# Optimization experiments

Hardware: AMD Instinct MI355X
Metric: run time of the kernel (lower is better)

Reference implementation:

```python
import jax, jax.numpy as jnp
import numpy as np

B, H, KV, HD, D, S = 8, 32, 8, 128, 4096, 4096
PAST = S - 2  # 4094, cache nearly full
ROPE_THETA = 10000.0


def rotate_half(x):
    h = x.shape[-1] // 2
    return jnp.concatenate([-x[..., h:], x[..., :h]], axis=-1)


def setup_inputs() -> dict:
    key = jax.random.key(0)
    ks = jax.random.split(key, 10)
    hidden_states = jax.random.normal(ks[0], (B, 1, D), jnp.float32)
    # HF additive causal mask for decode: 0 where position is valid, -inf-ish beyond
    pos = jnp.arange(S)
    attention_mask = jnp.broadcast_to(
        jnp.where(pos < PAST + 1, 0.0, -1e9).astype(jnp.float32)[None, None, None, :],
        (B, 1, 1, S),
    )
    # RoPE cos/sin for the single decoded position (position id = PAST)
    inv_freq = 1.0 / (ROPE_THETA ** (jnp.arange(0, HD, 2, dtype=jnp.float32) / HD))
    ang = PAST * inv_freq  # [HD/2]
    emb = jnp.concatenate([ang, ang], axis=-1)  # [HD]
    cos = jnp.broadcast_to(jnp.cos(emb)[None, None, :], (B, 1, HD)).astype(jnp.float32)
    sin = jnp.broadcast_to(jnp.sin(emb)[None, None, :], (B, 1, HD)).astype(jnp.float32)
    past_key = jax.random.normal(ks[1], (B, KV, PAST, HD), jnp.float32)
    past_value = jax.random.normal(ks[2], (B, KV, PAST, HD), jnp.float32)
    k_cache = jax.random.normal(ks[3], (B, KV, S, HD), jnp.float32)
    v_cache = jax.random.normal(ks[4], (B, KV, S, HD), jnp.float32)
    Wq = jax.random.normal(ks[5], (D, H * HD), jnp.float32) * 0.02
    Wk = jax.random.normal(ks[6], (D, KV * HD), jnp.float32) * 0.02
    Wv = jax.random.normal(ks[7], (D, KV * HD), jnp.float32) * 0.02
    Wo = jax.random.normal(ks[8], (H * HD, D), jnp.float32) * 0.02
    return dict(hidden_states=hidden_states, attention_mask=attention_mask, cos=cos,
                sin=sin, past_key=past_key, past_value=past_value,
                k_cache=k_cache, v_cache=v_cache, Wq=Wq, Wk=Wk, Wv=Wv, Wo=Wo)


def reference(hidden_states, attention_mask, cos, sin, past_key, past_value,
              k_cache, v_cache, Wq, Wk, Wv, Wo):
    b = hidden_states.shape[0]
    past_len = past_key.shape[2]  # static
    # q/k/v projections for the single decode token
    q = (hidden_states @ Wq).reshape(b, 1, H, HD).transpose(0, 2, 1, 3)   # [B,H,1,hd]
    k = (hidden_states @ Wk).reshape(b, 1, KV, HD).transpose(0, 2, 1, 3)  # [B,KV,1,hd]
    v = (hidden_states @ Wv).reshape(b, 1, KV, HD).transpose(0, 2, 1, 3)
    # rotary: cos/sin [B,1,hd] -> unsqueeze head dim -> [B,1,1,hd]
    c = cos[:, None, :, :]
    s = sin[:, None, :, :]
    q = q * c + rotate_half(q) * s
    k = k * c + rotate_half(k) * s
    # StaticCache: scatter past K/V into positions [0, past_len), new token at past_len
    kf = k_cache.at[:, :, :past_len, :].set(past_key)
    kf = kf.at[:, :, past_len:past_len + 1, :].set(k)
    vf = v_cache.at[:, :, :past_len, :].set(past_value)
    vf = vf.at[:, :, past_len:past_len + 1, :].set(v)
    # GQA: repeat kv heads
    n_rep = H // KV
    kr = jnp.repeat(kf, n_rep, axis=1)  # [B,H,S,hd]
    vr = jnp.repeat(vf, n_rep, axis=1)
    scores = jnp.einsum('bhqd,bhkd->bhqk', q, kr) / np.float32(np.sqrt(HD))
    scores = scores + attention_mask  # [B,1,1,S] broadcasts over heads
    probs = jax.nn.softmax(scores.astype(jnp.float32), axis=-1).astype(q.dtype)
    out = jnp.einsum('bhqk,bhkd->bhqd', probs, vr)  # [B,H,1,hd]
    out = out.transpose(0, 2, 1, 3).reshape(b, 1, H * HD)
    return out @ Wo  # [B,1,D]
```

## Files before the change

kernel.cpp:

```cpp
#include <hip/hip_runtime.h>

#define BB 8
#define HH 32
#define KVH 8
#define HD 128
#define DD 4096
#define PAST 4094
#define QCOLS 4096
#define KVCOLS 1024
#define NC_QKV 6144
#define DCH 64
#define NDCH 64
#define CHUNK 64
#define NCHUNK 64
#define QSCALE 0.08838834764831845f

__global__ __launch_bounds__(256)
void matvec_partial(const float* __restrict__ hin,
                    const float* __restrict__ W0,
                    const float* __restrict__ W1,
                    const float* __restrict__ W2,
                    int c_w1, int c_w2, int NC,
                    float* __restrict__ part)
{
    __shared__ float hl[DCH][BB];
    const int tid = threadIdx.x;
    const int d0 = blockIdx.y * DCH;
    const int cb = blockIdx.x * 512;

    for (int idx = tid; idx < DCH * BB; idx += 256) {
        int dd = idx & (DCH - 1);
        int b = idx >> 6;
        hl[dd][b] = hin[b * DD + d0 + dd];
    }
    __syncthreads();

    const int c = cb + tid * 2;
    const float* W;
    int ldw, cl;
    if (c < c_w1)      { W = W0; ldw = c_w1;        cl = c; }
    else if (c < c_w2) { W = W1; ldw = c_w2 - c_w1; cl = c - c_w1; }
    else               { W = W2; ldw = NC - c_w2;   cl = c - c_w2; }
    const float* wp = W + (size_t)d0 * ldw + cl;

    float2 acc[BB];
    #pragma unroll
    for (int b = 0; b < BB; ++b) { acc[b].x = 0.f; acc[b].y = 0.f; }

    #pragma unroll 8
    for (int dd = 0; dd < DCH; ++dd) {
        float2 w = *(const float2*)wp;
        wp += ldw;
        float hv[8];
        *(float4*)&hv[0] = *(const float4*)&hl[dd][0];
        *(float4*)&hv[4] = *(const float4*)&hl[dd][4];
        #pragma unroll
        for (int b = 0; b < BB; ++b) {
            acc[b].x = fmaf(hv[b], w.x, acc[b].x);
            acc[b].y = fmaf(hv[b], w.y, acc[b].y);
        }
    }

    float* po = part + (size_t)blockIdx.y * (BB * NC) + c;
    #pragma unroll
    for (int b = 0; b < BB; ++b) {
        *(float2*)(po + (size_t)b * NC) = acc[b];
    }
}

#define FIN_PER_B 3584
__global__ __launch_bounds__(256)
void qkv_finish(const float* __restrict__ part,
                const float* __restrict__ cosv,
                const float* __restrict__ sinv,
                float* __restrict__ qout,
                float* __restrict__ knew,
                float* __restrict__ vnew)
{
    const int idx = blockIdx.x * 256 + threadIdx.x;
    const int b = idx / FIN_PER_B;
    const int r = idx - b * FIN_PER_B;

    if (r < 2560) {
        const int hd = r & 63;
        const int head = r >> 6;
        const int c_lo = head * HD + hd;
        const float* p0 = part + (size_t)b * NC_QKV + c_lo;
        const float* p1 = p0 + 64;
        float s_lo = 0.f, s_hi = 0.f;
        #pragma unroll 8
        for (int i = 0; i < NDCH; ++i) {
            s_lo += p0[(size_t)i * (BB * NC_QKV)];
            s_hi += p1[(size_t)i * (BB * NC_QKV)];
        }
        const float cs_lo = cosv[b * HD + hd];
        const float sn_lo = sinv[b * HD + hd];
        const float cs_hi = cosv[b * HD + hd + 64];
        const float sn_hi = sinv[b * HD + hd + 64];
        const float v_lo = fmaf(s_lo, cs_lo, -s_hi * sn_lo);
        const float v_hi = fmaf(s_hi, cs_hi,  s_lo * sn_hi);
        if (c_lo < QCOLS) {
            qout[b * QCOLS + c_lo]      = v_lo * QSCALE;
            qout[b * QCOLS + c_lo + 64] = v_hi * QSCALE;
        } else {
            knew[b * KVCOLS + (c_lo - QCOLS)]      = v_lo;
            knew[b * KVCOLS + (c_lo - QCOLS) + 64] = v_hi;
        }
    } else {
        const int c = r - 2560 + QCOLS + KVCOLS;
        const float* p = part + (size_t)b * NC_QKV + c;
        float s = 0.f;
        #pragma unroll 8
        for (int i = 0; i < NDCH; ++i) s += p[(size_t)i * (BB * NC_QKV)];
        vnew[b * KVCOLS + (c - QCOLS - KVCOLS)] = s;
    }
}

__global__ __launch_bounds__(256)
void attn_partial(const float* __restrict__ past_key,
                  const float* __restrict__ past_value,
                  const float* __restrict__ q,
                  const float* __restrict__ knew,
                  const float* __restrict__ vnew,
                  float* __restrict__ pacc,
                  float* __restrict__ pl)
{
    const int pair = blockIdx.x;
    const int wid = threadIdx.x >> 6;
    const int chunk = blockIdx.y * 4 + wid;
    const int b = pair >> 3;
    const int kv = pair & 7;
    const int lane = threadIdx.x & 63;
    const int half = lane >> 5;
    const int lh = lane & 31;

    const float* qb = q + b * QCOLS + (kv * 4) * HD + 4 * lh;
    const float4 qv0 = *(const float4*)(qb);
    const float4 qv1 = *(const float4*)(qb + HD);
    const float4 qv2 = *(const float4*)(qb + 2 * HD);
    const float4 qv3 = *(const float4*)(qb + 3 * HD);

    const float* kb = past_key   + (size_t)pair * PAST * HD;
    const float* vb = past_value + (size_t)pair * PAST * HD;

    float4 acc0 = {0,0,0,0}, acc1 = {0,0,0,0}, acc2 = {0,0,0,0}, acc3 = {0,0,0,0};
    float l0 = 0.f, l1 = 0.f, l2 = 0.f, l3 = 0.f;

    const int jbase = chunk * CHUNK + half;

    if (chunk < NCHUNK - 1) {
        const float* kp = kb + (size_t)jbase * HD + 4 * lh;
        const float* vp = vb + (size_t)jbase * HD + 4 * lh;
        #pragma unroll 4
        for (int it = 0; it < 32; ++it) {
            const float4 kk = *(const float4*)kp;  kp += 2 * HD;
            float s0 = kk.x*qv0.x + kk.y*qv0.y + kk.z*qv0.z + kk.w*qv0.w;
            float s1 = kk.x*qv1.x + kk.y*qv1.y + kk.z*qv1.z + kk.w*qv1.w;
            float s2 = kk.x*qv2.x + kk.y*qv2.y + kk.z*qv2.z + kk.w*qv2.w;
            float s3 = kk.x*qv3.x + kk.y*qv3.y + kk.z*qv3.z + kk.w*qv3.w;
            #pragma unroll
            for (int m = 1; m <= 16; m <<= 1) {
                s0 += __shfl_xor(s0, m, 64);
                s1 += __shfl_xor(s1, m, 64);
                s2 += __shfl_xor(s2, m, 64);
                s3 += __shfl_xor(s3, m, 64);
            }
            const float4 vv = *(const float4*)vp;  vp += 2 * HD;
            const float p0 = __expf(s0);
            const float p1 = __expf(s1);
            const float p2 = __expf(s2);
            const float p3 = __expf(s3);
            l0 += p0; l1 += p1; l2 += p2; l3 += p3;
            acc0.x = fmaf(p0, vv.x, acc0.x); acc0.y = fmaf(p0, vv.y, acc0.y);
            acc0.z = fmaf(p0, vv.z, acc0.z); acc0.w = fmaf(p0, vv.w, acc0.w);
            acc1.x = fmaf(p1, vv.x, acc1.x); acc1.y = fmaf(p1, vv.y, acc1.y);
            acc1.z = fmaf(p1, vv.z, acc1.z); acc1.w = fmaf(p1, vv.w, acc1.w);
            acc2.x = fmaf(p2, vv.x, acc2.x); acc2.y = fmaf(p2, vv.y, acc2.y);
            acc2.z = fmaf(p2, vv.z, acc2.z); acc2.w = fmaf(p2, vv.w, acc2.w);
            acc3.x = fmaf(p3, vv.x, acc3.x); acc3.y = fmaf(p3, vv.y, acc3.y);
            acc3.z = fmaf(p3, vv.z, acc3.z); acc3.w = fmaf(p3, vv.w, acc3.w);
        }
    } else {
        const float* kn = knew + pair * HD;
        const float* vn = vnew + pair * HD;
        #pragma unroll 2
        for (int it = 0; it < 32; ++it) {
            const int j = jbase + it * 2;
            const bool valid = (j <= PAST);
            const float* kp;
            const float* vp;
            if (j < PAST) { kp = kb + (size_t)j * HD; vp = vb + (size_t)j * HD; }
            else          { kp = kn;                   vp = vn; }

            const float4 kk = *(const float4*)(kp + 4 * lh);
            float s0 = kk.x*qv0.x + kk.y*qv0.y + kk.z*qv0.z + kk.w*qv0.w;
            float s1 = kk.x*qv1.x + kk.y*qv1.y + kk.z*qv1.z + kk.w*qv1.w;
            float s2 = kk.x*qv2.x + kk.y*qv2.y + kk.z*qv2.z + kk.w*qv2.w;
            float s3 = kk.x*qv3.x + kk.y*qv3.y + kk.z*qv3.z + kk.w*qv3.w;
            #pragma unroll
            for (int m = 1; m <= 16; m <<= 1) {
                s0 += __shfl_xor(s0, m, 64);
                s1 += __shfl_xor(s1, m, 64);
                s2 += __shfl_xor(s2, m, 64);
                s3 += __shfl_xor(s3, m, 64);
            }
            const float4 vv = *(const float4*)(vp + 4 * lh);
            const float p0 = valid ? __expf(s0) : 0.f;
            const float p1 = valid ? __expf(s1) : 0.f;
            const float p2 = valid ? __expf(s2) : 0.f;
            const float p3 = valid ? __expf(s3) : 0.f;
            l0 += p0; l1 += p1; l2 += p2; l3 += p3;
            acc0.x = fmaf(p0, vv.x, acc0.x); acc0.y = fmaf(p0, vv.y, acc0.y);
            acc0.z = fmaf(p0, vv.z, acc0.z); acc0.w = fmaf(p0, vv.w, acc0.w);
            acc1.x = fmaf(p1, vv.x, acc1.x); acc1.y = fmaf(p1, vv.y, acc1.y);
            acc1.z = fmaf(p1, vv.z, acc1.z); acc1.w = fmaf(p1, vv.w, acc1.w);
            acc2.x = fmaf(p2, vv.x, acc2.x); acc2.y = fmaf(p2, vv.y, acc2.y);
            acc2.z = fmaf(p2, vv.z, acc2.z); acc2.w = fmaf(p2, vv.w, acc2.w);
            acc3.x = fmaf(p3, vv.x, acc3.x); acc3.y = fmaf(p3, vv.y, acc3.y);
            acc3.z = fmaf(p3, vv.z, acc3.z); acc3.w = fmaf(p3, vv.w, acc3.w);
        }
    }

    l0 += __shfl_xor(l0, 32, 64);
    l1 += __shfl_xor(l1, 32, 64);
    l2 += __shfl_xor(l2, 32, 64);
    l3 += __shfl_xor(l3, 32, 64);
    acc0.x += __shfl_xor(acc0.x, 32, 64); acc0.y += __shfl_xor(acc0.y, 32, 64);
    acc0.z += __shfl_xor(acc0.z, 32, 64); acc0.w += __shfl_xor(acc0.w, 32, 64);
    acc1.x += __shfl_xor(acc1.x, 32, 64); acc1.y += __shfl_xor(acc1.y, 32, 64);
    acc1.z += __shfl_xor(acc1.z, 32, 64); acc1.w += __shfl_xor(acc1.w, 32, 64);
    acc2.x += __shfl_xor(acc2.x, 32, 64); acc2.y += __shfl_xor(acc2.y, 32, 64);
    acc2.z += __shfl_xor(acc2.z, 32, 64); acc2.w += __shfl_xor(acc2.w, 32, 64);
    acc3.x += __shfl_xor(acc3.x, 32, 64); acc3.y += __shfl_xor(acc3.y, 32, 64);
    acc3.z += __shfl_xor(acc3.z, 32, 64); acc3.w += __shfl_xor(acc3.w, 32, 64);

    if (half == 0) {
        float* po = pacc + (((size_t)pair * NCHUNK + chunk) * 4) * HD + 4 * lh;
        *(float4*)(po)          = acc0;
        *(float4*)(po + HD)     = acc1;
        *(float4*)(po + 2*HD)   = acc2;
        *(float4*)(po + 3*HD)   = acc3;
        if (lh == 0) {
            float* plo = pl + ((size_t)pair * NCHUNK + chunk) * 4;
            plo[0] = l0; plo[1] = l1; plo[2] = l2; plo[3] = l3;
        }
    }
}

__global__ __launch_bounds__(256)
void attn_combine(const float* __restrict__ pacc,
                  const float* __restrict__ pl,
                  float* __restrict__ attn_out)
{
    const int idx = blockIdx.x * 256 + threadIdx.x;
    const int d = idx & 127;
    const int h = (idx >> 7) & 31;
    const int b = idx >> 12;
    const int kv = h >> 2;
    const int qi = h & 3;
    const int pair = b * 8 + kv;

    const float* pa  = pacc + (((size_t)pair * NCHUNK) * 4 + qi) * HD + d;
    const float* pls = pl + (size_t)pair * NCHUNK * 4 + qi;
    float acc = 0.f, lsum = 0.f;
    #pragma unroll 8
    for (int c = 0; c < NCHUNK; ++c) {
        acc  += pa[(size_t)c * 4 * HD];
        lsum += pls[c * 4];
    }
    attn_out[b * QCOLS + h * HD + d] = acc / lsum;
}

__global__ __launch_bounds__(256)
void wo_finish(const float* __restrict__ part, float* __restrict__ out)
{
    const int idx = blockIdx.x * 256 + threadIdx.x;
    float s = 0.f;
    #pragma unroll 8
    for (int i = 0; i < NDCH; ++i) s += part[(size_t)i * (BB * QCOLS) + idx];
    out[idx] = s;
}

extern "C" void kernel_launch(void* const* d_in, const int* in_sizes, int n_in,
                              void* d_out, int out_size, void* d_ws, size_t ws_size,
                              hipStream_t stream)
{
    (void)in_sizes; (void)n_in; (void)out_size; (void)ws_size;
    const float* hidden     = (const float*)d_in[0];
    const float* cosv       = (const float*)d_in[2];
    const float* sinv       = (const float*)d_in[3];
    const float* past_key   = (const float*)d_in[4];
    const float* past_value = (const float*)d_in[5];
    const float* Wq = (const float*)d_in[8];
    const float* Wk = (const float*)d_in[9];
    const float* Wv = (const float*)d_in[10];
    const float* Wo = (const float*)d_in[11];
    float* out = (float*)d_out;
    float* ws  = (float*)d_ws;

    float* qkv_part = ws;
    float* qrope    = qkv_part + (size_t)NDCH * BB * NC_QKV;
    float* knew     = qrope + BB * QCOLS;
    float* vnew     = knew + BB * KVCOLS;
    float* pacc     = vnew + BB * KVCOLS;
    float* pl       = pacc + (size_t)64 * NCHUNK * 4 * HD;
    float* attn_out = pl + (size_t)64 * NCHUNK * 4;
    float* wo_part  = qkv_part;

    matvec_partial<<<dim3(12, NDCH), 256, 0, stream>>>(
        hidden, Wq, Wk, Wv, 4096, 5120, NC_QKV, qkv_part);
    qkv_finish<<<(BB * FIN_PER_B) / 256, 256, 0, stream>>>(
        qkv_part, cosv, sinv, qrope, knew, vnew);
    attn_partial<<<dim3(64, NCHUNK / 4), 256, 0, stream>>>(
        past_key, past_value, qrope, knew, vnew, pacc, pl);
    attn_combine<<<(BB * HH * HD) / 256, 256, 0, stream>>>(pacc, pl, attn_out);
    matvec_partial<<<dim3(8, NDCH), 256, 0, stream>>>(
        attn_out, Wo, Wo, Wo, 4096, 5120, QCOLS, wo_part);
    wo_finish<<<(BB * QCOLS) / 256, 256, 0, stream>>>(wo_part, out);
}
```

Measured before the change: 111.7 us.

## Halve matvec split-K chunks, DPP reductions, in-block attention chunk combine, vectorized finish

Doubles the D-chunk per matvec block, which halves the number of split-K partials written and re-read. It replaces the shfl_xor reductions in the attention kernel with DPP/swizzle intrinsics. Each attention block now reduces its four wavefront chunks in shared memory before writing one partial, which shrinks the combine pass. wo_finish is vectorized to float4. The costs are fewer matvec blocks in flight, which lowers parallelism, and a new __syncthreads in the attention kernel.

```diff
diff --git a/kernel.cpp b/kernel.cpp
--- a/kernel.cpp
+++ b/kernel.cpp
@@ -9,11 +9,26 @@
 #define QCOLS 4096
 #define KVCOLS 1024
 #define NC_QKV 6144
-#define DCH 64
-#define NDCH 64
+#define DCH 128
+#define NDCH 32
 #define CHUNK 64
-#define NCHUNK 64
+#define YCH 16
 #define QSCALE 0.08838834764831845f
+
+__device__ __forceinline__ float sum32(float x) {
+    int t;
+    t = __builtin_amdgcn_update_dpp(0, __float_as_int(x), 0x121, 0xf, 0xf, false);
+    x += __int_as_float(t);
+    t = __builtin_amdgcn_update_dpp(0, __float_as_int(x), 0x122, 0xf, 0xf, false);
+    x += __int_as_float(t);
+    t = __builtin_amdgcn_update_dpp(0, __float_as_int(x), 0x124, 0xf, 0xf, false);
+    x += __int_as_float(t);
+    t = __builtin_amdgcn_update_dpp(0, __float_as_int(x), 0x128, 0xf, 0xf, false);
+    x += __int_as_float(t);
+    t = __builtin_amdgcn_ds_swizzle(__float_as_int(x), 0x401F);
+    x += __int_as_float(t);
+    return x;
+}
 
 __global__ __launch_bounds__(256)
 void matvec_partial(const float* __restrict__ hin,
@@ -30,7 +45,7 @@
 
     for (int idx = tid; idx < DCH * BB; idx += 256) {
         int dd = idx & (DCH - 1);
-        int b = idx >> 6;
+        int b = idx >> 7;
         hl[dd][b] = hin[b * DD + d0 + dd];
     }
     __syncthreads();
@@ -47,7 +62,7 @@
     #pragma unroll
     for (int b = 0; b < BB; ++b) { acc[b].x = 0.f; acc[b].y = 0.f; }
 
-    #pragma unroll 8
+    #pragma unroll 16
     for (int dd = 0; dd < DCH; ++dd) {
         float2 w = *(const float2*)wp;
         wp += ldw;
@@ -148,7 +163,7 @@
 
     const int jbase = chunk * CHUNK + half;
 
-    if (chunk < NCHUNK - 1) {
+    if (chunk < 63) {
         const float* kp = kb + (size_t)jbase * HD + 4 * lh;
         const float* vp = vb + (size_t)jbase * HD + 4 * lh;
         #pragma unroll 4
@@ -158,13 +173,7 @@
             float s1 = kk.x*qv1.x + kk.y*qv1.y + kk.z*qv1.z + kk.w*qv1.w;
             float s2 = kk.x*qv2.x + kk.y*qv2.y + kk.z*qv2.z + kk.w*qv2.w;
             float s3 = kk.x*qv3.x + kk.y*qv3.y + kk.z*qv3.z + kk.w*qv3.w;
-            #pragma unroll
-            for (int m = 1; m <= 16; m <<= 1) {
-                s0 += __shfl_xor(s0, m, 64);
-                s1 += __shfl_xor(s1, m, 64);
-                s2 += __shfl_xor(s2, m, 64);
-                s3 += __shfl_xor(s3, m, 64);
-            }
+            s0 = sum32(s0); s1 = sum32(s1); s2 = sum32(s2); s3 = sum32(s3);
             const float4 vv = *(const float4*)vp;  vp += 2 * HD;
             const float p0 = __expf(s0);
             const float p1 = __expf(s1);
@@ -197,13 +206,7 @@
             float s1 = kk.x*qv1.x + kk.y*qv1.y + kk.z*qv1.z + kk.w*qv1.w;
             float s2 = kk.x*qv2.x + kk.y*qv2.y + kk.z*qv2.z + kk.w*qv2.w;
             float s3 = kk.x*qv3.x + kk.y*qv3.y + kk.z*qv3.z + kk.w*qv3.w;
-            #pragma unroll
-            for (int m = 1; m <= 16; m <<= 1) {
-                s0 += __shfl_xor(s0, m, 64);
-                s1 += __shfl_xor(s1, m, 64);
-                s2 += __shfl_xor(s2, m, 64);
-                s3 += __shfl_xor(s3, m, 64);
-            }
+            s0 = sum32(s0); s1 = sum32(s1); s2 = sum32(s2); s3 = sum32(s3);
             const float4 vv = *(const float4*)(vp + 4 * lh);
             const float p0 = valid ? __expf(s0) : 0.f;
             const float p1 = valid ? __expf(s1) : 0.f;
@@ -234,16 +237,29 @@
     acc3.x += __shfl_xor(acc3.x, 32, 64); acc3.y += __shfl_xor(acc3.y, 32, 64);
     acc3.z += __shfl_xor(acc3.z, 32, 64); acc3.w += __shfl_xor(acc3.w, 32, 64);
 
+    __shared__ float lacc[4][4][HD];
+    __shared__ float ll[4][4];
     if (half == 0) {
-        float* po = pacc + (((size_t)pair * NCHUNK + chunk) * 4) * HD + 4 * lh;
-        *(float4*)(po)          = acc0;
-        *(float4*)(po + HD)     = acc1;
-        *(float4*)(po + 2*HD)   = acc2;
-        *(float4*)(po + 3*HD)   = acc3;
+        *(float4*)&lacc[wid][0][4 * lh] = acc0;
+        *(float4*)&lacc[wid][1][4 * lh] = acc1;
+        *(float4*)&lacc[wid][2][4 * lh] = acc2;
+        *(float4*)&lacc[wid][3][4 * lh] = acc3;
         if (lh == 0) {
-            float* plo = pl + ((size_t)pair * NCHUNK + chunk) * 4;
-            plo[0] = l0; plo[1] = l1; plo[2] = l2; plo[3] = l3;
-        }
+            ll[wid][0] = l0; ll[wid][1] = l1; ll[wid][2] = l2; ll[wid][3] = l3;
+        }
+    }
+    __syncthreads();
+    const int d2 = lane * 2;
+    float ax = lacc[0][wid][d2]     + lacc[1][wid][d2]
+             + lacc[2][wid][d2]     + lacc[3][wid][d2];
+    float ay = lacc[0][wid][d2 + 1] + lacc[1][wid][d2 + 1]
+             + lacc[2][wid][d2 + 1] + lacc[3][wid][d2 + 1];
+    float* po = pacc + (((size_t)pair * YCH + blockIdx.y) * 4 + wid) * HD + d2;
+    float2 r; r.x = ax; r.y = ay;
+    *(float2*)po = r;
+    if (lane == 0) {
+        pl[((size_t)pair * YCH + blockIdx.y) * 4 + wid] =
+            ll[0][wid] + ll[1][wid] + ll[2][wid] + ll[3][wid];
     }
 }
 
@@ -260,11 +276,11 @@
     const int qi = h & 3;
     const int pair = b * 8 + kv;
 
-    const float* pa  = pacc + (((size_t)pair * NCHUNK) * 4 + qi) * HD + d;
-    const float* pls = pl + (size_t)pair * NCHUNK * 4 + qi;
+    const float* pa  = pacc + ((size_t)pair * YCH * 4 + qi) * HD + d;
+    const float* pls = pl + (size_t)pair * YCH * 4 + qi;
     float acc = 0.f, lsum = 0.f;
     #pragma unroll 8
-    for (int c = 0; c < NCHUNK; ++c) {
+    for (int c = 0; c < YCH; ++c) {
         acc  += pa[(size_t)c * 4 * HD];
         lsum += pls[c * 4];
     }
@@ -275,10 +291,14 @@
 void wo_finish(const float* __restrict__ part, float* __restrict__ out)
 {
     const int idx = blockIdx.x * 256 + threadIdx.x;
-    float s = 0.f;
+    const float* p = part + (size_t)idx * 4;
+    float4 s = {0.f, 0.f, 0.f, 0.f};
     #pragma unroll 8
-    for (int i = 0; i < NDCH; ++i) s += part[(size_t)i * (BB * QCOLS) + idx];
-    out[idx] = s;
+    for (int i = 0; i < NDCH; ++i) {
+        const float4 t = *(const float4*)(p + (size_t)i * (BB * QCOLS));
+        s.x += t.x; s.y += t.y; s.z += t.z; s.w += t.w;
+    }
+    *(float4*)(out + (size_t)idx * 4) = s;
 }
 
 extern "C" void kernel_launch(void* const* d_in, const int* in_sizes, int n_in,
@@ -303,18 +323,18 @@
     float* knew     = qrope + BB * QCOLS;
     float* vnew     = knew + BB * KVCOLS;
     float* pacc     = vnew + BB * KVCOLS;
-    float* pl       = pacc + (size_t)64 * NCHUNK * 4 * HD;
-    float* attn_out = pl + (size_t)64 * NCHUNK * 4;
+    float* pl       = pacc + (size_t)64 * YCH * 4 * HD;
+    float* attn_out = pl + (size_t)64 * YCH * 4;
     float* wo_part  = qkv_part;
 
     matvec_partial<<<dim3(12, NDCH), 256, 0, stream>>>(
         hidden, Wq, Wk, Wv, 4096, 5120, NC_QKV, qkv_part);
     qkv_finish<<<(BB * FIN_PER_B) / 256, 256, 0, stream>>>(
         qkv_part, cosv, sinv, qrope, knew, vnew);
-    attn_partial<<<dim3(64, NCHUNK / 4), 256, 0, stream>>>(
+    attn_partial<<<dim3(64, YCH), 256, 0, stream>>>(
         past_key, past_value, qrope, knew, vnew, pacc, pl);
     attn_combine<<<(BB * HH * HD) / 256, 256, 0, stream>>>(pacc, pl, attn_out);
     matvec_partial<<<dim3(8, NDCH), 256, 0, stream>>>(
         attn_out, Wo, Wo, Wo, 4096, 5120, QCOLS, wo_part);
-    wo_finish<<<(BB * QCOLS) / 256, 256, 0, stream>>>(wo_part, out);
-}
+    wo_finish<<<(BB * QCOLS / 4) / 256, 256, 0, stream>>>(wo_part, out);
+}
```

After: 126.5 us. +13.2%, slower.
